# Kernel optimization log

Hardware: AMD Instinct MI355X
Metric: run time of the kernel (lower is better)

The kernel has to match this reference:

```python
import jax, jax.numpy as jnp
import numpy as np

B = 1_000_000   # collocation points
N = 64          # layers[1]: number of tiny identity-init linear+activation layers
D = 3           # layers[0]: per-layer feature dim (rho, p, u columns)


def setup_inputs() -> dict:
    key = jax.random.key(0)
    k_x, k_w, k_cr, k_cp, k_cu = jax.random.split(key, 5)
    x = jax.random.normal(k_x, (B, D), dtype=jnp.float32)
    # Per-layer weights: identity init (as in the module) plus small noise so
    # the N layers are not all identical in the test harness.
    eye = jnp.eye(D, dtype=jnp.float32)
    W = eye[None, :, :] + 0.01 * jax.random.normal(k_w, (N, D, D), dtype=jnp.float32)
    b = jnp.zeros((N, D), dtype=jnp.float32)
    # Frozen output heads (Linear(N, 1, bias=False)), all initialized from c_initial.
    c_rho = jax.random.normal(k_cr, (1, N), dtype=jnp.float32)
    c_p = jax.random.normal(k_cp, (1, N), dtype=jnp.float32)
    c_u = jax.random.normal(k_cu, (1, N), dtype=jnp.float32)
    return {"x": x, "W": W, "b": b, "c_rho": c_rho, "c_p": c_p, "c_u": c_u}


def reference(x, W, b, c_rho, c_p, c_u):
    # Original loop: for i in range(N): u = act(Linear_i(x)); gather columns 0,1,2
    # and iteratively torch.cat them. Vectorized: one batched tiny GEMM over all
    # N layers, then slice the three channels.
    # x: [B, D]; W: [N, D, D]; b: [N, D] -> u: [B, N, D]
    u = jnp.tanh(jnp.einsum('bd,nkd->bnk', x, W) + b[None, :, :])
    u_rho = u[:, :, 0]   # [B, N]
    u_p = u[:, :, 1]
    u_u = u[:, :, 2]
    out_rho = u_rho @ c_rho.T   # [B, 1]
    out_p = u_p @ c_p.T
    out_u = u_u @ c_u.T
    return (out_rho, out_p, out_u)
```

## Files before the change

### kernel.cpp

```cpp
#include <hip/hip_runtime.h>


#define NN   64
#define RPT  4
#define BLK  256

__device__ __forceinline__ float fast_exp2(float x) {
#if __has_builtin(__builtin_amdgcn_exp2f)
    return __builtin_amdgcn_exp2f(x);
#else
    return exp2f(x);
#endif
}

__device__ __forceinline__ float fast_rcp(float x) {
#if __has_builtin(__builtin_amdgcn_rcpf)
    return __builtin_amdgcn_rcpf(x);
#else
    return 1.0f / x;
#endif
}

__device__ __forceinline__ float fast_tanh(float x) {
    float e = fast_exp2(x * 2.8853900817779268f);
    float r = fast_rcp(e + 1.0f);
    return fmaf(-2.0f, r, 1.0f);
}

__global__ __launch_bounds__(BLK) void fused_tanh_heads(
    const float* __restrict__ x,
    const float* __restrict__ W,
    const float* __restrict__ bias,
    const float* __restrict__ c_rho,
    const float* __restrict__ c_p,
    const float* __restrict__ c_u,
    float* __restrict__ out,
    int B)
{
    __shared__ float sc[NN * 16];
    const int t = threadIdx.x;
    if (t < NN) {
        #pragma unroll
        for (int j = 0; j < 9; ++j) sc[t * 16 + j] = W[t * 9 + j];
        #pragma unroll
        for (int k = 0; k < 3; ++k) sc[t * 16 + 9 + k] = bias[t * 3 + k];
        sc[t * 16 + 12] = c_rho[t];
        sc[t * 16 + 13] = c_p[t];
        sc[t * 16 + 14] = c_u[t];
        sc[t * 16 + 15] = 0.0f;
    }
    __syncthreads();

    const int base = blockIdx.x * (BLK * RPT);

    float xr[RPT][3];
    int   rows[RPT];
    #pragma unroll
    for (int i = 0; i < RPT; ++i) {
        const int r = base + i * BLK + t;
        rows[i] = r;
        const bool ok = (r < B);
        xr[i][0] = ok ? x[r * 3 + 0] : 0.0f;
        xr[i][1] = ok ? x[r * 3 + 1] : 0.0f;
        xr[i][2] = ok ? x[r * 3 + 2] : 0.0f;
    }

    float acc[RPT][3];
    #pragma unroll
    for (int i = 0; i < RPT; ++i) {
        acc[i][0] = 0.0f; acc[i][1] = 0.0f; acc[i][2] = 0.0f;
    }

    const float4* scv = (const float4*)sc;
    #pragma unroll 4
    for (int n = 0; n < NN; ++n) {
        const float4 q0 = scv[n * 4 + 0];
        const float4 q1 = scv[n * 4 + 1];
        const float4 q2 = scv[n * 4 + 2];
        const float4 q3 = scv[n * 4 + 3];
        #pragma unroll
        for (int i = 0; i < RPT; ++i) {
            const float x0 = xr[i][0], x1 = xr[i][1], x2 = xr[i][2];
            float h0 = fmaf(x2, q0.z, fmaf(x1, q0.y, fmaf(x0, q0.x, q2.y)));
            float h1 = fmaf(x2, q1.y, fmaf(x1, q1.x, fmaf(x0, q0.w, q2.z)));
            float h2 = fmaf(x2, q2.x, fmaf(x1, q1.w, fmaf(x0, q1.z, q2.w)));
            const float t0 = fast_tanh(h0);
            const float t1 = fast_tanh(h1);
            const float t2 = fast_tanh(h2);
            acc[i][0] = fmaf(t0, q3.x, acc[i][0]);
            acc[i][1] = fmaf(t1, q3.y, acc[i][1]);
            acc[i][2] = fmaf(t2, q3.z, acc[i][2]);
        }
    }

    #pragma unroll
    for (int i = 0; i < RPT; ++i) {
        const int r = rows[i];
        if (r < B) {
            out[r]         = acc[i][0];
            out[B + r]     = acc[i][1];
            out[2 * B + r] = acc[i][2];
        }
    }
}

extern "C" void kernel_launch(void* const* d_in, const int* in_sizes, int n_in,
                              void* d_out, int out_size, void* d_ws, size_t ws_size,
                              hipStream_t stream) {
    (void)d_ws; (void)ws_size; (void)n_in; (void)out_size;
    const float* x     = (const float*)d_in[0];
    const float* W     = (const float*)d_in[1];
    const float* bias  = (const float*)d_in[2];
    const float* c_rho = (const float*)d_in[3];
    const float* c_p   = (const float*)d_in[4];
    const float* c_u   = (const float*)d_in[5];
    float* out = (float*)d_out;

    const int B = in_sizes[0] / 3;
    const int rows_per_block = BLK * RPT;
    const int grid = (B + rows_per_block - 1) / rows_per_block;

    fused_tanh_heads<<<grid, BLK, 0, stream>>>(x, W, bias, c_rho, c_p, c_u, out, B);
}
```

Measured before the change: 128.7 us.

## Use packed FMA on row pairs and share reciprocals across three tanh

The kernel now processes two rows per thread as packed float2 lanes and uses v_pk_fma for the affine, tanh-finish and head-accumulate steps. The tanh scale constant is folded into the weights and bias in shared memory, and those values are duplicated so they load as pairs. Three reciprocals per row are replaced by one via a Montgomery-style batched inverse. This is meant to cut VALU instruction count on a compute-bound transcendental loop, in exchange for more LDS traffic per layer, fewer rows per thread, and a possible overflow in the product of three exp terms.

Result: faster. 113.3 us (-12.0%).

```diff
diff --git a/kernel.cpp b/kernel.cpp
--- a/kernel.cpp
+++ b/kernel.cpp
@@ -2,29 +2,27 @@
 
 
 #define NN   64
-#define RPT  4
+#define RPT  2
 #define BLK  256
 
-__device__ __forceinline__ float fast_exp2(float x) {
+typedef float f2 __attribute__((ext_vector_type(2)));
+
+__device__ __forceinline__ f2 mk2(float a, float b) { f2 r; r.x = a; r.y = b; return r; }
+__device__ __forceinline__ f2 pkfma(f2 a, f2 b, f2 c) { return __builtin_elementwise_fma(a, b, c); }
+
+__device__ __forceinline__ float fexp2(float x) {
 #if __has_builtin(__builtin_amdgcn_exp2f)
     return __builtin_amdgcn_exp2f(x);
 #else
     return exp2f(x);
 #endif
 }
-
-__device__ __forceinline__ float fast_rcp(float x) {
+__device__ __forceinline__ float frcp(float x) {
 #if __has_builtin(__builtin_amdgcn_rcpf)
     return __builtin_amdgcn_rcpf(x);
 #else
     return 1.0f / x;
 #endif
-}
-
-__device__ __forceinline__ float fast_tanh(float x) {
-    float e = fast_exp2(x * 2.8853900817779268f);
-    float r = fast_rcp(e + 1.0f);
-    return fmaf(-2.0f, r, 1.0f);
 }
 
 __global__ __launch_bounds__(BLK) void fused_tanh_heads(
@@ -37,70 +35,96 @@
     float* __restrict__ out,
     int B)
 {
-    __shared__ float sc[NN * 16];
+    __shared__ float sc[NN * 32];
     const int t = threadIdx.x;
     if (t < NN) {
+        const float K = 2.8853900817779268f;
+        float* rec = &sc[t * 32];
         #pragma unroll
-        for (int j = 0; j < 9; ++j) sc[t * 16 + j] = W[t * 9 + j];
+        for (int j = 0; j < 9; ++j) {
+            const float w = W[t * 9 + j] * K;
+            rec[2 * j] = w; rec[2 * j + 1] = w;
+        }
         #pragma unroll
-        for (int k = 0; k < 3; ++k) sc[t * 16 + 9 + k] = bias[t * 3 + k];
-        sc[t * 16 + 12] = c_rho[t];
-        sc[t * 16 + 13] = c_p[t];
-        sc[t * 16 + 14] = c_u[t];
-        sc[t * 16 + 15] = 0.0f;
+        for (int k = 0; k < 3; ++k) {
+            const float bb = bias[t * 3 + k] * K;
+            rec[18 + 2 * k] = bb; rec[19 + 2 * k] = bb;
+        }
+        const float cr = c_rho[t], cp = c_p[t], cu = c_u[t];
+        rec[24] = cr; rec[25] = cr;
+        rec[26] = cp; rec[27] = cp;
+        rec[28] = cu; rec[29] = cu;
+        rec[30] = 0.0f; rec[31] = 0.0f;
     }
     __syncthreads();
 
-    const int base = blockIdx.x * (BLK * RPT);
+    const int r0 = blockIdx.x * (BLK * RPT) + t;
+    const int r1 = r0 + BLK;
+    const bool ok0 = (r0 < B), ok1 = (r1 < B);
 
-    float xr[RPT][3];
-    int   rows[RPT];
-    #pragma unroll
-    for (int i = 0; i < RPT; ++i) {
-        const int r = base + i * BLK + t;
-        rows[i] = r;
-        const bool ok = (r < B);
-        xr[i][0] = ok ? x[r * 3 + 0] : 0.0f;
-        xr[i][1] = ok ? x[r * 3 + 1] : 0.0f;
-        xr[i][2] = ok ? x[r * 3 + 2] : 0.0f;
+    const f2 X0 = mk2(ok0 ? x[r0 * 3 + 0] : 0.0f, ok1 ? x[r1 * 3 + 0] : 0.0f);
+    const f2 X1 = mk2(ok0 ? x[r0 * 3 + 1] : 0.0f, ok1 ? x[r1 * 3 + 1] : 0.0f);
+    const f2 X2 = mk2(ok0 ? x[r0 * 3 + 2] : 0.0f, ok1 ? x[r1 * 3 + 2] : 0.0f);
+
+    f2 acc0 = mk2(0.0f, 0.0f), acc1 = acc0, acc2 = acc0;
+    const f2 neg2 = mk2(-2.0f, -2.0f), one2 = mk2(1.0f, 1.0f);
+
+    const float4* q4 = (const float4*)sc;
+    #pragma unroll 2
+    for (int n = 0; n < NN; ++n) {
+        const float4 Q0 = q4[n * 8 + 0];
+        const float4 Q1 = q4[n * 8 + 1];
+        const float4 Q2 = q4[n * 8 + 2];
+        const float4 Q3 = q4[n * 8 + 3];
+        const float4 Q4 = q4[n * 8 + 4];
+        const float4 Q5 = q4[n * 8 + 5];
+        const float4 Q6 = q4[n * 8 + 6];
+        const float4 Q7 = q4[n * 8 + 7];
+
+        f2 h0 = pkfma(X2, mk2(Q1.x, Q1.y),
+                 pkfma(X1, mk2(Q0.z, Q0.w),
+                  pkfma(X0, mk2(Q0.x, Q0.y), mk2(Q4.z, Q4.w))));
+        f2 h1 = pkfma(X2, mk2(Q2.z, Q2.w),
+                 pkfma(X1, mk2(Q2.x, Q2.y),
+                  pkfma(X0, mk2(Q1.z, Q1.w), mk2(Q5.x, Q5.y))));
+        f2 h2 = pkfma(X2, mk2(Q4.x, Q4.y),
+                 pkfma(X1, mk2(Q3.z, Q3.w),
+                  pkfma(X0, mk2(Q3.x, Q3.y), mk2(Q5.z, Q5.w))));
+
+        const float a00 = fexp2(h0.x) + 1.0f, a01 = fexp2(h0.y) + 1.0f;
+        const float a10 = fexp2(h1.x) + 1.0f, a11 = fexp2(h1.y) + 1.0f;
+        const float a20 = fexp2(h2.x) + 1.0f, a21 = fexp2(h2.y) + 1.0f;
+
+        const float m0  = a00 * a10;
+        const float rA  = frcp(m0 * a20);
+        const float i20 = m0 * rA;
+        const float s0  = a20 * rA;
+        const float i00 = a10 * s0;
+        const float i10 = a00 * s0;
+        const float m1  = a01 * a11;
+        const float rB  = frcp(m1 * a21);
+        const float i21 = m1 * rB;
+        const float s1  = a21 * rB;
+        const float i01 = a11 * s1;
+        const float i11 = a01 * s1;
+
+        const f2 T0 = pkfma(neg2, mk2(i00, i01), one2);
+        const f2 T1 = pkfma(neg2, mk2(i10, i11), one2);
+        const f2 T2 = pkfma(neg2, mk2(i20, i21), one2);
+        acc0 = pkfma(T0, mk2(Q6.x, Q6.y), acc0);
+        acc1 = pkfma(T1, mk2(Q6.z, Q6.w), acc1);
+        acc2 = pkfma(T2, mk2(Q7.x, Q7.y), acc2);
     }
 
-    float acc[RPT][3];
-    #pragma unroll
-    for (int i = 0; i < RPT; ++i) {
-        acc[i][0] = 0.0f; acc[i][1] = 0.0f; acc[i][2] = 0.0f;
+    if (ok0) {
+        out[r0]         = acc0.x;
+        out[B + r0]     = acc1.x;
+        out[2 * B + r0] = acc2.x;
     }
-
-    const float4* scv = (const float4*)sc;
-    #pragma unroll 4
-    for (int n = 0; n < NN; ++n) {
-        const float4 q0 = scv[n * 4 + 0];
-        const float4 q1 = scv[n * 4 + 1];
-        const float4 q2 = scv[n * 4 + 2];
-        const float4 q3 = scv[n * 4 + 3];
-        #pragma unroll
-        for (int i = 0; i < RPT; ++i) {
-            const float x0 = xr[i][0], x1 = xr[i][1], x2 = xr[i][2];
-            float h0 = fmaf(x2, q0.z, fmaf(x1, q0.y, fmaf(x0, q0.x, q2.y)));
-            float h1 = fmaf(x2, q1.y, fmaf(x1, q1.x, fmaf(x0, q0.w, q2.z)));
-            float h2 = fmaf(x2, q2.x, fmaf(x1, q1.w, fmaf(x0, q1.z, q2.w)));
-            const float t0 = fast_tanh(h0);
-            const float t1 = fast_tanh(h1);
-            const float t2 = fast_tanh(h2);
-            acc[i][0] = fmaf(t0, q3.x, acc[i][0]);
-            acc[i][1] = fmaf(t1, q3.y, acc[i][1]);
-            acc[i][2] = fmaf(t2, q3.z, acc[i][2]);
-        }
-    }
-
-    #pragma unroll
-    for (int i = 0; i < RPT; ++i) {
-        const int r = rows[i];
-        if (r < B) {
-            out[r]         = acc[i][0];
-            out[B + r]     = acc[i][1];
-            out[2 * B + r] = acc[i][2];
-        }
+    if (ok1) {
+        out[r1]         = acc0.y;
+        out[B + r1]     = acc1.y;
+        out[2 * B + r1] = acc2.y;
     }
 }
 
```

## Fold tanh constants into weights and share one reciprocal across three channels

Applied to the files above, without the earlier changes.

The 2/ln2 scale is folded into the weights and bias when they are staged in shared memory, which removes one multiply per activation. Because sum(c*(1-2r)) equals sum(c) minus 2*sum(c*r), the head sums are computed once by a wavefront reduction and applied at store time, so the loop accumulates only c*r. The three reciprocals per row and layer are replaced by a single reciprocal of their product plus a few multiplies, trading transcendental throughput for extra VALU work. Risk: the product of three exp terms can overflow to inf for large pre-activations, giving zero or NaN where separate reciprocals would have been fine.

Result: faster. 126.1 us (-2.1%).

```diff
diff --git a/kernel.cpp b/kernel.cpp
--- a/kernel.cpp
+++ b/kernel.cpp
@@ -5,26 +5,19 @@
 #define RPT  4
 #define BLK  256
 
-__device__ __forceinline__ float fast_exp2(float x) {
+__device__ __forceinline__ float fexp2(float x) {
 #if __has_builtin(__builtin_amdgcn_exp2f)
     return __builtin_amdgcn_exp2f(x);
 #else
     return exp2f(x);
 #endif
 }
-
-__device__ __forceinline__ float fast_rcp(float x) {
+__device__ __forceinline__ float frcp(float x) {
 #if __has_builtin(__builtin_amdgcn_rcpf)
     return __builtin_amdgcn_rcpf(x);
 #else
     return 1.0f / x;
 #endif
-}
-
-__device__ __forceinline__ float fast_tanh(float x) {
-    float e = fast_exp2(x * 2.8853900817779268f);
-    float r = fast_rcp(e + 1.0f);
-    return fmaf(-2.0f, r, 1.0f);
 }
 
 __global__ __launch_bounds__(BLK) void fused_tanh_heads(
@@ -39,57 +32,74 @@
 {
     __shared__ float sc[NN * 16];
     const int t = threadIdx.x;
-    if (t < NN) {
-        #pragma unroll
-        for (int j = 0; j < 9; ++j) sc[t * 16 + j] = W[t * 9 + j];
-        #pragma unroll
-        for (int k = 0; k < 3; ++k) sc[t * 16 + 9 + k] = bias[t * 3 + k];
-        sc[t * 16 + 12] = c_rho[t];
-        sc[t * 16 + 13] = c_p[t];
-        sc[t * 16 + 14] = c_u[t];
-        sc[t * 16 + 15] = 0.0f;
+    #pragma unroll
+    for (int k = 0; k < 4; ++k) {
+        const int idx = t + BLK * k;
+        const int n = idx >> 4;
+        const int o = idx & 15;
+        const float K = 2.8853900817779268f;
+        float v;
+        if (o < 9)       v = W[n * 9 + o] * K;
+        else if (o < 12) v = bias[n * 3 + (o - 9)] * K;
+        else if (o == 12) v = c_rho[n];
+        else if (o == 13) v = c_p[n];
+        else if (o == 14) v = c_u[n];
+        else              v = 0.0f;
+        sc[idx] = v;
     }
     __syncthreads();
 
-    const int base = blockIdx.x * (BLK * RPT);
+    float C0 = c_rho[t & 63], C1 = c_p[t & 63], C2 = c_u[t & 63];
+    #pragma unroll
+    for (int o = 1; o < 64; o <<= 1) {
+        C0 += __shfl_xor(C0, o);
+        C1 += __shfl_xor(C1, o);
+        C2 += __shfl_xor(C2, o);
+    }
 
-    float xr[RPT][3];
+    const int base = blockIdx.x * (BLK * RPT) + t;
+
     int   rows[RPT];
+    float xs[RPT][3];
     #pragma unroll
     for (int i = 0; i < RPT; ++i) {
-        const int r = base + i * BLK + t;
+        const int r = base + i * BLK;
         rows[i] = r;
         const bool ok = (r < B);
-        xr[i][0] = ok ? x[r * 3 + 0] : 0.0f;
-        xr[i][1] = ok ? x[r * 3 + 1] : 0.0f;
-        xr[i][2] = ok ? x[r * 3 + 2] : 0.0f;
+        xs[i][0] = ok ? x[r * 3 + 0] : 0.0f;
+        xs[i][1] = ok ? x[r * 3 + 1] : 0.0f;
+        xs[i][2] = ok ? x[r * 3 + 2] : 0.0f;
     }
 
     float acc[RPT][3];
     #pragma unroll
-    for (int i = 0; i < RPT; ++i) {
-        acc[i][0] = 0.0f; acc[i][1] = 0.0f; acc[i][2] = 0.0f;
-    }
+    for (int i = 0; i < RPT; ++i) { acc[i][0] = acc[i][1] = acc[i][2] = 0.0f; }
 
-    const float4* scv = (const float4*)sc;
-    #pragma unroll 4
+    const float4* q4 = (const float4*)sc;
+    #pragma unroll 2
     for (int n = 0; n < NN; ++n) {
-        const float4 q0 = scv[n * 4 + 0];
-        const float4 q1 = scv[n * 4 + 1];
-        const float4 q2 = scv[n * 4 + 2];
-        const float4 q3 = scv[n * 4 + 3];
+        const float4 q0 = q4[n * 4 + 0];
+        const float4 q1 = q4[n * 4 + 1];
+        const float4 q2 = q4[n * 4 + 2];
+        const float4 q3 = q4[n * 4 + 3];
         #pragma unroll
         for (int i = 0; i < RPT; ++i) {
-            const float x0 = xr[i][0], x1 = xr[i][1], x2 = xr[i][2];
-            float h0 = fmaf(x2, q0.z, fmaf(x1, q0.y, fmaf(x0, q0.x, q2.y)));
-            float h1 = fmaf(x2, q1.y, fmaf(x1, q1.x, fmaf(x0, q0.w, q2.z)));
-            float h2 = fmaf(x2, q2.x, fmaf(x1, q1.w, fmaf(x0, q1.z, q2.w)));
-            const float t0 = fast_tanh(h0);
-            const float t1 = fast_tanh(h1);
-            const float t2 = fast_tanh(h2);
-            acc[i][0] = fmaf(t0, q3.x, acc[i][0]);
-            acc[i][1] = fmaf(t1, q3.y, acc[i][1]);
-            acc[i][2] = fmaf(t2, q3.z, acc[i][2]);
+            const float x0 = xs[i][0], x1 = xs[i][1], x2 = xs[i][2];
+            const float h0 = fmaf(x2, q0.z, fmaf(x1, q0.y, fmaf(x0, q0.x, q2.y)));
+            const float h1 = fmaf(x2, q1.y, fmaf(x1, q1.x, fmaf(x0, q0.w, q2.z)));
+            const float h2 = fmaf(x2, q2.x, fmaf(x1, q1.w, fmaf(x0, q1.z, q2.w)));
+            const float a0 = fexp2(h0) + 1.0f;
+            const float a1 = fexp2(h1) + 1.0f;
+            const float a2 = fexp2(h2) + 1.0f;
+            const float m  = a0 * a1;
+            const float rr = frcp(m * a2);
+            const float i2 = m  * rr;
+            const float s  = a2 * rr;
+            const float i0 = a1 * s;
+            const float i1 = a0 * s;
+            acc[i][0] = fmaf(i0, q3.x, acc[i][0]);
+            acc[i][1] = fmaf(i1, q3.y, acc[i][1]);
+            acc[i][2] = fmaf(i2, q3.z, acc[i][2]);
         }
     }
 
@@ -97,9 +107,9 @@
     for (int i = 0; i < RPT; ++i) {
         const int r = rows[i];
         if (r < B) {
-            out[r]         = acc[i][0];
-            out[B + r]     = acc[i][1];
-            out[2 * B + r] = acc[i][2];
+            out[r]         = fmaf(-2.0f, acc[i][0], C0);
+            out[B + r]     = fmaf(-2.0f, acc[i][1], C1);
+            out[2 * B + r] = fmaf(-2.0f, acc[i][2], C2);
         }
     }
 }
```
